# Kernel optimization log

Measured on AMD Instinct MI355X. Metric: run time of the kernel, lower is better.

Reference implementation:

```python
import jax, jax.numpy as jnp
import numpy as np

B, S, IN, OUT, P = 4, 1024, 128, 128, 16
CTX = min(IN, OUT)
MAX_SEQ = 4096


def setup_inputs() -> dict:
    key = jax.random.key(0)
    keys = iter(jax.random.split(key, 32))
    nk = lambda: next(keys)

    def linear(fi, fo):
        lim = 1.0 / np.sqrt(fi)
        W = jax.random.uniform(nk(), (fi, fo), jnp.float32, -lim, lim)
        b = jax.random.uniform(nk(), (fo,), jnp.float32, -lim, lim)
        return W, b

    x = jax.random.normal(nk(), (B, S, IN), jnp.float32)
    context_features = jax.random.normal(nk(), (B, S, CTX), jnp.float32)
    flow_patterns = jax.random.normal(nk(), (P, OUT, IN), jnp.float32) * 0.1
    w_sel1, b_sel1 = linear(IN + CTX, 2 * P)
    w_sel2, b_sel2 = linear(2 * P, P)
    w_int1, b_int1 = linear(IN + CTX, 64)
    w_int2, b_int2 = linear(64, 1)
    w_win1, b_win1 = linear(IN, 64)
    w_win2, b_win2 = linear(64, 1)
    return dict(x=x, context_features=context_features, flow_patterns=flow_patterns,
                w_sel1=w_sel1, b_sel1=b_sel1, w_sel2=w_sel2, b_sel2=b_sel2,
                w_int1=w_int1, b_int1=b_int1, w_int2=w_int2, b_int2=b_int2,
                w_win1=w_win1, b_win1=b_win1, w_win2=w_win2, b_win2=b_win2)


def _gelu(v):
    return jax.nn.gelu(v, approximate=False)  # torch nn.GELU default (erf)


def reference(x, context_features, flow_patterns,
              w_sel1, b_sel1, w_sel2, b_sel2,
              w_int1, b_int1, w_int2, b_int2,
              w_win1, b_win1, w_win2, b_win2):
    # combined input [B,S,IN+CTX]
    combined = jnp.concatenate([x, context_features], axis=-1)
    # pattern weights [B,S,P]
    pattern_weights = jax.nn.softmax(_gelu(combined @ w_sel1 + b_sel1) @ w_sel2 + b_sel2, axis=-1)
    # per-token flow matrix [B,S,OUT,IN]
    flow = jnp.einsum('bsp,poi->bsoi', pattern_weights, flow_patterns)
    # flow intensity [B,S,1] -> [B,S,1,1]
    intensity = jax.nn.sigmoid(_gelu(combined @ w_int1 + b_int1) @ w_int2 + b_int2)
    flow = flow * intensity[..., None]
    # adaptive window size [B,1]
    window_size = jax.nn.sigmoid(_gelu(x.mean(axis=1) @ w_win1 + b_win1) @ w_win2 + b_win2)
    window_size = window_size * (MAX_SEQ - 256) + 256
    # context-aware topk sparsity over flattened out*in dim
    adaptive_sparsity = 0.1 * jnp.mean(window_size / MAX_SEQ)  # scalar
    D = OUT * IN
    k = jnp.maximum(1, jnp.floor(D * adaptive_sparsity)).astype(jnp.int32)
    flat = flow.reshape(B, S, D)
    a = jnp.abs(flat)
    sorted_a = jnp.sort(a, axis=-1)  # ascending
    # k-th largest abs value per (b,s) row; k is a traced scalar -> dynamic_slice
    thr = jax.lax.dynamic_slice_in_dim(sorted_a, D - k, 1, axis=-1)  # [B,S,1]
    mask = jax.lax.stop_gradient((a >= thr).astype(flat.dtype))
    return (mask * flat).reshape(B, S, OUT, IN)
```

## Files before the change

kernel.cpp:

```cpp
#include <hip/hip_runtime.h>
#include <math.h>

#define S_   1024
#define D_   16384
#define CAPL 512
#define NB   512

typedef float v4f __attribute__((ext_vector_type(4)));

__device__ __forceinline__ double gelu64(double v) {
    return 0.5 * v * (1.0 + erf(v * 0.70710678118654752440));
}
__device__ __forceinline__ float gelu32(float v) {
    return 0.5f * v * (1.0f + erff(v * 0.70710678f));
}
__device__ __forceinline__ double sigmoid64(double z) {
    return 1.0 / (1.0 + exp(-z));
}
__device__ __forceinline__ float sigmoid32(float z) {
    return 1.0f / (1.0f + expf(-z));
}
__device__ __forceinline__ float rfl(float x) {
    return __uint_as_float(__builtin_amdgcn_readfirstlane(__float_as_uint(x)));
}

__global__ __launch_bounds__(256) void mlp_kernel(
    const float* __restrict__ x, const float* __restrict__ ctx,
    const float* __restrict__ w_sel1, const float* __restrict__ b_sel1,
    const float* __restrict__ w_sel2, const float* __restrict__ b_sel2,
    const float* __restrict__ w_int1, const float* __restrict__ b_int1,
    const float* __restrict__ w_int2, const float* __restrict__ b_int2,
    double* __restrict__ pw64, float* __restrict__ pw32,
    double* __restrict__ it64, float* __restrict__ it32)
{
    __shared__ double comb[2][256];
    __shared__ double h1[2][32];
    __shared__ float ipart[2][2];
    const int tid = threadIdx.x;
    const int tok0 = blockIdx.x * 2;
    const int t = tid >> 7, local = tid & 127;

    for (int r = 0; r < 2; ++r) {
        int idx = tid + r * 256;
        int tk = idx >> 8, i = idx & 255;
        comb[tk][i] = (double)((i < 128) ? x[(tok0 + tk) * 128 + i]
                                         : ctx[(tok0 + tk) * 128 + (i - 128)]);
    }
    __syncthreads();

    {
        int u = local >> 2, sl = local & 3;
        int i0 = sl * 64;
        double s0 = (sl == 0) ? (double)b_sel1[u] : 0.0, s1 = 0.0;
        for (int i = 0; i < 64; i += 2) {
            s0 = fma(comb[t][i0 + i],     (double)w_sel1[(i0 + i) * 32 + u],     s0);
            s1 = fma(comb[t][i0 + i + 1], (double)w_sel1[(i0 + i + 1) * 32 + u], s1);
        }
        double s = s0 + s1;
        s += __shfl_xor(s, 1);
        s += __shfl_xor(s, 2);
        if (sl == 0) h1[t][u] = gelu64(s);
    }
    {
        int u = local >> 1, sl = local & 1;
        int i0 = sl * 128;
        float a0 = (sl == 0) ? b_int1[u] : 0.0f, a1 = 0.0f, a2 = 0.0f, a3 = 0.0f;
        for (int i = 0; i < 128; i += 4) {
            a0 = fmaf((float)comb[t][i0 + i],     w_int1[(i0 + i) * 64 + u],     a0);
            a1 = fmaf((float)comb[t][i0 + i + 1], w_int1[(i0 + i + 1) * 64 + u], a1);
            a2 = fmaf((float)comb[t][i0 + i + 2], w_int1[(i0 + i + 2) * 64 + u], a2);
            a3 = fmaf((float)comb[t][i0 + i + 3], w_int1[(i0 + i + 3) * 64 + u], a3);
        }
        float s = (a0 + a1) + (a2 + a3);
        s += __shfl_xor(s, 1);
        float val = (sl == 0) ? gelu32(s) * w_int2[u] : 0.0f;
        for (int off = 2; off <= 32; off <<= 1)
            val += __shfl_xor(val, off);
        val += __shfl_xor(val, 1);
        if ((local & 63) == 0) ipart[t][local >> 6] = val;
    }
    __syncthreads();

    if (tid < 32) {
        int t2 = tid >> 4, u = tid & 15;
        double z = (double)b_sel2[u];
        for (int j = 0; j < 32; ++j)
            z = fma(h1[t2][j], (double)w_sel2[j * 16 + u], z);
        double m = z;
        for (int off = 8; off >= 1; off >>= 1) m = fmax(m, __shfl_xor(m, off));
        double e = exp(z - m);
        double ssum = e;
        for (int off = 8; off >= 1; off >>= 1) ssum += __shfl_xor(ssum, off);
        double pwv = e / ssum;
        pw64[(tok0 + t2) * 16 + u] = pwv;
        pw32[(tok0 + t2) * 16 + u] = (float)pwv;
    } else if (tid < 34) {
        int t3 = tid - 32;
        float iv = sigmoid32(ipart[t3][0] + ipart[t3][1] + b_int2[0]);
        it64[tok0 + t3] = (double)iv;
        it32[tok0 + t3] = iv;
    }
}

__global__ __launch_bounds__(256) void win_part_kernel(
    const float* __restrict__ x, double* __restrict__ wpart)
{
    __shared__ double red[2][128];
    const int tid = threadIdx.x;
    const int b = blockIdx.x >> 4, chunk = blockIdx.x & 15;
    int i = tid & 127, h = tid >> 7;
    double a0 = 0.0, a1 = 0.0;
    int s0 = b * S_ + chunk * 64 + h * 32;
    for (int j = 0; j < 32; j += 2) {
        a0 += (double)x[(s0 + j) * 128 + i];
        a1 += (double)x[(s0 + j + 1) * 128 + i];
    }
    red[h][i] = a0 + a1;
    __syncthreads();
    if (tid < 128)
        wpart[(b * 16 + chunk) * 128 + tid] = red[0][tid] + red[1][tid];
}

__global__ __launch_bounds__(256) void win_fin_kernel(
    const double* __restrict__ wpart,
    const float* __restrict__ w_win1, const float* __restrict__ b_win1,
    const float* __restrict__ w_win2, const float* __restrict__ b_win2,
    double* __restrict__ win_out)
{
    __shared__ double xm[4][128];
    const int tid = threadIdx.x;
    const int b = tid >> 6, lane = tid & 63;
    for (int r = 0; r < 2; ++r) {
        int i = lane + r * 64;
        double s = 0.0;
        for (int c = 0; c < 16; ++c)
            s += wpart[(b * 16 + c) * 128 + i];
        xm[b][i] = s * (1.0 / 1024.0);
    }
    __syncthreads();
    {
        int u = lane;
        double s0 = (double)b_win1[u], s1 = 0.0;
        for (int i = 0; i < 128; i += 2) {
            s0 = fma(xm[b][i],     (double)w_win1[i * 64 + u],       s0);
            s1 = fma(xm[b][i + 1], (double)w_win1[(i + 1) * 64 + u], s1);
        }
        double c = gelu64(s0 + s1) * (double)w_win2[u];
        for (int off = 32; off >= 1; off >>= 1) c += __shfl_xor(c, off);
        if (lane == 0)
            win_out[b] = sigmoid64(c + (double)b_win2[0]) * 3840.0 + 256.0;
    }
}

__global__ __launch_bounds__(512, 4) void flow_kernel(
    const float* __restrict__ patterns,
    const double* __restrict__ pw64, const float* __restrict__ pw32,
    const double* __restrict__ it64, const float* __restrict__ it32,
    const double* __restrict__ win,
    float* __restrict__ out)
{
    __shared__ unsigned hist[2][NB];
    __shared__ unsigned flagBits[2][512];
    __shared__ unsigned listIdx[2][CAPL];
    __shared__ double listVal[2][CAPL];
    __shared__ float smax[2][8];
    __shared__ int sred[8];
    __shared__ int bcastB[2];
    __shared__ unsigned listCnt[2];

    const int tid = threadIdx.x;
    const int lane = tid & 63, wv = tid >> 6;
    const int t0 = blockIdx.x * 2, t1 = t0 + 1;

    for (int r = tid; r < 2 * NB; r += 512) hist[r >> 9][r & (NB - 1)] = 0;
    for (int r = tid; r < 1024; r += 512) flagBits[r >> 9][r & 511] = 0;
    if (tid < 2) listCnt[tid] = 0;

    double w0 = win[0] * (1.0 / 4096.0), w1 = win[1] * (1.0 / 4096.0);
    double w2 = win[2] * (1.0 / 4096.0), w3 = win[3] * (1.0 / 4096.0);
    double mean = (((w0 + w1) + w2) + w3) * 0.25;
    double kd = floor(16384.0 * (0.1 * mean));
    int k = (kd < 1.0) ? 1 : (int)kd;

    float qw0[16], qw1[16];
#pragma unroll
    for (int p = 0; p < 16; ++p) {
        qw0[p] = rfl(pw32[t0 * 16 + p]);
        qw1[p] = rfl(pw32[t1 * 16 + p]);
    }
    float i0 = rfl(it32[t0]), i1 = rfl(it32[t1]);

    const v4f* pat4 = (const v4f*)patterns;
    v4f v0[8], v1[8];
#pragma unroll
    for (int c = 0; c < 8; ++c) {
        int grp = c * 512 + tid;
        v4f a0 = (v4f)(0.0f), a1 = (v4f)(0.0f);
        v4f pp[8];
#pragma unroll
        for (int p = 0; p < 8; ++p) pp[p] = pat4[p * 4096 + grp];
#pragma unroll
        for (int p = 0; p < 8; ++p) { a0 += qw0[p] * pp[p]; a1 += qw1[p] * pp[p]; }
#pragma unroll
        for (int p = 0; p < 8; ++p) pp[p] = pat4[(8 + p) * 4096 + grp];
#pragma unroll
        for (int p = 0; p < 8; ++p) { a0 += qw0[8 + p] * pp[p]; a1 += qw1[8 + p] * pp[p]; }
        v0[c] = a0 * i0;
        v1[c] = a1 * i1;
    }

    float mx0 = 0.0f, mx1 = 0.0f;
#pragma unroll
    for (int c = 0; c < 8; ++c) {
        mx0 = fmaxf(mx0, fmaxf(fmaxf(fabsf(v0[c].x), fabsf(v0[c].y)),
                               fmaxf(fabsf(v0[c].z), fabsf(v0[c].w))));
        mx1 = fmaxf(mx1, fmaxf(fmaxf(fabsf(v1[c].x), fabsf(v1[c].y)),
                               fmaxf(fabsf(v1[c].z), fabsf(v1[c].w))));
    }
    for (int off = 32; off >= 1; off >>= 1) {
        mx0 = fmaxf(mx0, __shfl_xor(mx0, off));
        mx1 = fmaxf(mx1, __shfl_xor(mx1, off));
    }
    if (lane == 0) { smax[0][wv] = mx0; smax[1][wv] = mx1; }
    __syncthreads();
    mx0 = smax[0][0]; mx1 = smax[1][0];
#pragma unroll
    for (int w = 1; w < 8; ++w) {
        mx0 = fmaxf(mx0, smax[0][w]);
        mx1 = fmaxf(mx1, smax[1][w]);
    }
    int base0 = (int)(__float_as_uint(mx0) >> 17) - (NB - 1);
    int base1 = (int)(__float_as_uint(mx1) >> 17) - (NB - 1);
    if (base0 < 0) base0 = 0;
    if (base1 < 0) base1 = 0;

#pragma unroll
    for (int c = 0; c < 8; ++c) {
#pragma unroll
        for (int q = 0; q < 4; ++q) {
            int b0 = (int)(__float_as_uint(fabsf(v0[c][q])) >> 17) - base0;
            if (b0 > 0) atomicAdd(&hist[0][b0 > NB - 1 ? NB - 1 : b0], 1u);
            int b1 = (int)(__float_as_uint(fabsf(v1[c][q])) >> 17) - base1;
            if (b1 > 0) atomicAdd(&hist[1][b1 > NB - 1 ? NB - 1 : b1], 1u);
        }
    }
    __syncthreads();

    if (wv < 2) {
        int t = wv;
        int sum8 = 0;
#pragma unroll
        for (int j = 0; j < 8; ++j) sum8 += (int)hist[t][lane * 8 + j];
        int suffix = sum8;
        for (int off = 1; off <= 32; off <<= 1) {
            int other = __shfl_down(suffix, off);
            if (lane + off < 64) suffix += other;
        }
        int sufNext = __shfl_down(suffix, 1);
        if (lane == 63) sufNext = 0;
        unsigned long long msk = __ballot(suffix >= k);
        int Lstar = (msk == 0) ? 0 : (63 - __clzll(msk));
        if (lane == Lstar) {
            int cnt = sufNext, B = Lstar * 8;
            for (int j = 7; j >= 0; --j) {
                cnt += (int)hist[t][Lstar * 8 + j];
                if (cnt >= k) { B = Lstar * 8 + j; break; }
            }
            bcastB[t] = B;
        }
    }
    __syncthreads();

    int B0 = bcastB[0], B1 = bcastB[1];
    float loF0 = (B0 + base0) ? __uint_as_float((unsigned)(B0 + base0) << 17) : 0.0f;
    float hiF0 = __uint_as_float((unsigned)(B0 + base0 + 1) << 17);
    float loF1 = (B1 + base1) ? __uint_as_float((unsigned)(B1 + base1) << 17) : 0.0f;
    float hiF1 = __uint_as_float((unsigned)(B1 + base1 + 1) << 17);

    float E0 = 3e-6f * i0, E1 = 3e-6f * i1;
    float loCut0 = loF0 - 2.0f * E0, hiCut0 = hiF0 + 2.0f * E0;
    float loCut1 = loF1 - 2.0f * E1, hiCut1 = hiF1 + 2.0f * E1;

    int ns0 = 0, ns1 = 0;
#pragma unroll
    for (int c = 0; c < 8; ++c) {
#pragma unroll
        for (int q = 0; q < 4; ++q) {
            unsigned e = (unsigned)(4 * (c * 512 + tid) + q);
            float a0 = fabsf(v0[c][q]);
            if (a0 >= hiCut0) ns0++;
            else if (a0 >= loCut0) {
                unsigned pos = atomicAdd(&listCnt[0], 1u);
                if (pos < CAPL) listIdx[0][pos] = e;
            }
            float a1 = fabsf(v1[c][q]);
            if (a1 >= hiCut1) ns1++;
            else if (a1 >= loCut1) {
                unsigned pos = atomicAdd(&listCnt[1], 1u);
                if (pos < CAPL) listIdx[1][pos] = e;
            }
        }
    }
    {
        int pk = ns0 | (ns1 << 16);
#pragma unroll
        for (int off = 32; off >= 1; off >>= 1) pk += __shfl_xor(pk, off);
        if (lane == 0) sred[wv] = pk;
    }
    __syncthreads();
    int tot = 0;
#pragma unroll
    for (int w = 0; w < 8; ++w) tot += sred[w];
    int m0 = k - (tot & 0xffff), m1 = k - (tot >> 16);
    int c0n = (int)(listCnt[0] < CAPL ? listCnt[0] : CAPL);
    int c1n = (int)(listCnt[1] < CAPL ? listCnt[1] : CAPL);

    double itt0 = it64[t0], itt1 = it64[t1];
    int totL = c0n + c1n;
    for (int g = tid; g < totL; g += 512) {
        int tk = (g >= c0n);
        int e = tk ? (g - c0n) : g;
        unsigned idx = listIdx[tk][e];
        const double* pwp = pw64 + (tk ? t1 : t0) * 16;
        double s = 0.0;
#pragma unroll
        for (int p = 0; p < 16; ++p)
            s = fma(pwp[p], (double)patterns[p * D_ + idx], s);
        listVal[tk][e] = fabs(s * (tk ? itt1 : itt0));
    }
    __syncthreads();
    for (int g = tid; g < totL; g += 512) {
        int tk = (g >= c0n);
        int e = tk ? (g - c0n) : g;
        double my = listVal[tk][e];
        int cnt = tk ? c1n : c0n, m = tk ? m1 : m0;
        int r = 0;
        for (int j = 0; j < cnt; ++j) r += (listVal[tk][j] > my);
        if (r < m) {
            unsigned idx = listIdx[tk][e];
            atomicOr(&flagBits[tk][idx >> 5], 1u << (idx & 31));
        }
    }
    __syncthreads();

    v4f* o0p = (v4f*)(out + (size_t)t0 * D_);
    v4f* o1p = (v4f*)(out + (size_t)t1 * D_);
#pragma unroll
    for (int c = 0; c < 8; ++c) {
        int grp = c * 512 + tid;
        v4f r0, r1;
#pragma unroll
        for (int q = 0; q < 4; ++q) {
            unsigned e = (unsigned)(4 * grp + q);
            float av = fabsf(v0[c][q]);
            bool keep = (av >= hiCut0);
            if (!keep && av >= loCut0) keep = (flagBits[0][e >> 5] >> (e & 31)) & 1u;
            r0[q] = keep ? v0[c][q] : 0.0f;
            av = fabsf(v1[c][q]);
            keep = (av >= hiCut1);
            if (!keep && av >= loCut1) keep = (flagBits[1][e >> 5] >> (e & 31)) & 1u;
            r1[q] = keep ? v1[c][q] : 0.0f;
        }
        __builtin_nontemporal_store(r0, &o0p[grp]);
        __builtin_nontemporal_store(r1, &o1p[grp]);
    }
}

extern "C" void kernel_launch(void* const* d_in, const int* in_sizes, int n_in,
                              void* d_out, int out_size, void* d_ws, size_t ws_size,
                              hipStream_t stream) {
    const float* x        = (const float*)d_in[0];
    const float* ctx      = (const float*)d_in[1];
    const float* patterns = (const float*)d_in[2];
    const float* w_sel1   = (const float*)d_in[3];
    const float* b_sel1   = (const float*)d_in[4];
    const float* w_sel2   = (const float*)d_in[5];
    const float* b_sel2   = (const float*)d_in[6];
    const float* w_int1   = (const float*)d_in[7];
    const float* b_int1   = (const float*)d_in[8];
    const float* w_int2   = (const float*)d_in[9];
    const float* b_int2   = (const float*)d_in[10];
    const float* w_win1   = (const float*)d_in[11];
    const float* b_win1   = (const float*)d_in[12];
    const float* w_win2   = (const float*)d_in[13];
    const float* b_win2   = (const float*)d_in[14];

    double* ws    = (double*)d_ws;
    double* win   = ws;
    double* pw64  = ws + 8;
    double* it64  = pw64 + 65536;
    double* wpart = it64 + 4096;
    float*  pw32  = (float*)(wpart + 8192);
    float*  it32  = pw32 + 65536;
    float*  out   = (float*)d_out;

    hipLaunchKernelGGL(mlp_kernel, dim3(2048), dim3(256), 0, stream,
                       x, ctx, w_sel1, b_sel1, w_sel2, b_sel2,
                       w_int1, b_int1, w_int2, b_int2, pw64, pw32, it64, it32);
    hipLaunchKernelGGL(win_part_kernel, dim3(64), dim3(256), 0, stream, x, wpart);
    hipLaunchKernelGGL(win_fin_kernel, dim3(1), dim3(256), 0, stream,
                       wpart, w_win1, b_win1, w_win2, b_win2, win);
    hipLaunchKernelGGL(flow_kernel, dim3(2048), dim3(512), 0, stream,
                       patterns, pw64, pw32, it64, it32, win, out);
}
```

Measured before the change: 441.3 us.

## Process four tokens per block in flow kernel to reuse pattern loads

The flow kernel now handles four tokens per block instead of two, so each pattern load is shared across four accumulations. This halves the grid and the total pattern-read traffic through cache. Register pressure doubles (four 32-element vectors per thread), so launch bounds drop to 2 blocks per CU. The refine stage now assumes each list fits in one pass of 512 threads, and the shared-memory footprint grows.

```diff
diff --git a/kernel.cpp b/kernel.cpp
--- a/kernel.cpp
+++ b/kernel.cpp
@@ -152,29 +152,29 @@
     }
 }
 
-__global__ __launch_bounds__(512, 4) void flow_kernel(
+__global__ __launch_bounds__(512, 2) void flow_kernel(
     const float* __restrict__ patterns,
     const double* __restrict__ pw64, const float* __restrict__ pw32,
     const double* __restrict__ it64, const float* __restrict__ it32,
     const double* __restrict__ win,
     float* __restrict__ out)
 {
-    __shared__ unsigned hist[2][NB];
-    __shared__ unsigned flagBits[2][512];
-    __shared__ unsigned listIdx[2][CAPL];
-    __shared__ double listVal[2][CAPL];
-    __shared__ float smax[2][8];
+    __shared__ unsigned hist[4][NB];
+    __shared__ unsigned flagBits[4][512];
+    __shared__ unsigned listIdx[4][CAPL];
+    __shared__ double listVal[4][CAPL];
+    __shared__ float smax[4][8];
     __shared__ int sred[8];
-    __shared__ int bcastB[2];
-    __shared__ unsigned listCnt[2];
+    __shared__ int bcastB[4];
+    __shared__ unsigned listCnt[4];
 
     const int tid = threadIdx.x;
     const int lane = tid & 63, wv = tid >> 6;
-    const int t0 = blockIdx.x * 2, t1 = t0 + 1;
-
-    for (int r = tid; r < 2 * NB; r += 512) hist[r >> 9][r & (NB - 1)] = 0;
-    for (int r = tid; r < 1024; r += 512) flagBits[r >> 9][r & 511] = 0;
-    if (tid < 2) listCnt[tid] = 0;
+    const int t0 = blockIdx.x * 4;
+
+    for (int r = tid; r < 4 * NB; r += 512) hist[r >> 9][r & (NB - 1)] = 0;
+    for (int r = tid; r < 2048; r += 512) flagBits[r >> 9][r & 511] = 0;
+    if (tid < 4) listCnt[tid] = 0;
 
     double w0 = win[0] * (1.0 / 4096.0), w1 = win[1] * (1.0 / 4096.0);
     double w2 = win[2] * (1.0 / 4096.0), w3 = win[3] * (1.0 / 4096.0);
@@ -182,71 +182,98 @@
     double kd = floor(16384.0 * (0.1 * mean));
     int k = (kd < 1.0) ? 1 : (int)kd;
 
-    float qw0[16], qw1[16];
+    float qw0[16], qw1[16], qw2[16], qw3[16];
 #pragma unroll
     for (int p = 0; p < 16; ++p) {
-        qw0[p] = rfl(pw32[t0 * 16 + p]);
-        qw1[p] = rfl(pw32[t1 * 16 + p]);
-    }
-    float i0 = rfl(it32[t0]), i1 = rfl(it32[t1]);
+        qw0[p] = rfl(pw32[(t0 + 0) * 16 + p]);
+        qw1[p] = rfl(pw32[(t0 + 1) * 16 + p]);
+        qw2[p] = pw32[(t0 + 2) * 16 + p];
+        qw3[p] = pw32[(t0 + 3) * 16 + p];
+    }
+    float it0 = rfl(it32[t0 + 0]), it1 = rfl(it32[t0 + 1]);
+    float it2 = it32[t0 + 2],      it3 = it32[t0 + 3];
 
     const v4f* pat4 = (const v4f*)patterns;
-    v4f v0[8], v1[8];
+    v4f v0[8], v1[8], v2[8], v3[8];
 #pragma unroll
     for (int c = 0; c < 8; ++c) {
         int grp = c * 512 + tid;
-        v4f a0 = (v4f)(0.0f), a1 = (v4f)(0.0f);
+        v4f a0 = (v4f)(0.0f), a1 = (v4f)(0.0f), a2 = (v4f)(0.0f), a3 = (v4f)(0.0f);
         v4f pp[8];
 #pragma unroll
         for (int p = 0; p < 8; ++p) pp[p] = pat4[p * 4096 + grp];
 #pragma unroll
-        for (int p = 0; p < 8; ++p) { a0 += qw0[p] * pp[p]; a1 += qw1[p] * pp[p]; }
+        for (int p = 0; p < 8; ++p) {
+            a0 += qw0[p] * pp[p]; a1 += qw1[p] * pp[p];
+            a2 += qw2[p] * pp[p]; a3 += qw3[p] * pp[p];
+        }
 #pragma unroll
         for (int p = 0; p < 8; ++p) pp[p] = pat4[(8 + p) * 4096 + grp];
 #pragma unroll
-        for (int p = 0; p < 8; ++p) { a0 += qw0[8 + p] * pp[p]; a1 += qw1[8 + p] * pp[p]; }
-        v0[c] = a0 * i0;
-        v1[c] = a1 * i1;
-    }
-
-    float mx0 = 0.0f, mx1 = 0.0f;
+        for (int p = 0; p < 8; ++p) {
+            a0 += qw0[8 + p] * pp[p]; a1 += qw1[8 + p] * pp[p];
+            a2 += qw2[8 + p] * pp[p]; a3 += qw3[8 + p] * pp[p];
+        }
+        v0[c] = a0 * it0; v1[c] = a1 * it1;
+        v2[c] = a2 * it2; v3[c] = a3 * it3;
+    }
+
+    float mx0 = 0.0f, mx1 = 0.0f, mx2 = 0.0f, mx3 = 0.0f;
 #pragma unroll
     for (int c = 0; c < 8; ++c) {
         mx0 = fmaxf(mx0, fmaxf(fmaxf(fabsf(v0[c].x), fabsf(v0[c].y)),
                                fmaxf(fabsf(v0[c].z), fabsf(v0[c].w))));
         mx1 = fmaxf(mx1, fmaxf(fmaxf(fabsf(v1[c].x), fabsf(v1[c].y)),
                                fmaxf(fabsf(v1[c].z), fabsf(v1[c].w))));
+        mx2 = fmaxf(mx2, fmaxf(fmaxf(fabsf(v2[c].x), fabsf(v2[c].y)),
+                               fmaxf(fabsf(v2[c].z), fabsf(v2[c].w))));
+        mx3 = fmaxf(mx3, fmaxf(fmaxf(fabsf(v3[c].x), fabsf(v3[c].y)),
+                               fmaxf(fabsf(v3[c].z), fabsf(v3[c].w))));
     }
     for (int off = 32; off >= 1; off >>= 1) {
         mx0 = fmaxf(mx0, __shfl_xor(mx0, off));
         mx1 = fmaxf(mx1, __shfl_xor(mx1, off));
-    }
-    if (lane == 0) { smax[0][wv] = mx0; smax[1][wv] = mx1; }
-    __syncthreads();
-    mx0 = smax[0][0]; mx1 = smax[1][0];
-#pragma unroll
-    for (int w = 1; w < 8; ++w) {
-        mx0 = fmaxf(mx0, smax[0][w]);
-        mx1 = fmaxf(mx1, smax[1][w]);
-    }
-    int base0 = (int)(__float_as_uint(mx0) >> 17) - (NB - 1);
-    int base1 = (int)(__float_as_uint(mx1) >> 17) - (NB - 1);
-    if (base0 < 0) base0 = 0;
-    if (base1 < 0) base1 = 0;
+        mx2 = fmaxf(mx2, __shfl_xor(mx2, off));
+        mx3 = fmaxf(mx3, __shfl_xor(mx3, off));
+    }
+    if (lane == 0) {
+        smax[0][wv] = mx0; smax[1][wv] = mx1;
+        smax[2][wv] = mx2; smax[3][wv] = mx3;
+    }
+    __syncthreads();
+    int base[4];
+    {
+        float m0 = smax[0][0], m1 = smax[1][0], m2 = smax[2][0], m3 = smax[3][0];
+#pragma unroll
+        for (int w = 1; w < 8; ++w) {
+            m0 = fmaxf(m0, smax[0][w]); m1 = fmaxf(m1, smax[1][w]);
+            m2 = fmaxf(m2, smax[2][w]); m3 = fmaxf(m3, smax[3][w]);
+        }
+        int b0 = (int)(__float_as_uint(m0) >> 17) - (NB - 1);
+        int b1 = (int)(__float_as_uint(m1) >> 17) - (NB - 1);
+        int b2 = (int)(__float_as_uint(m2) >> 17) - (NB - 1);
+        int b3 = (int)(__float_as_uint(m3) >> 17) - (NB - 1);
+        base[0] = (b0 < 0) ? 0 : b0; base[1] = (b1 < 0) ? 0 : b1;
+        base[2] = (b2 < 0) ? 0 : b2; base[3] = (b3 < 0) ? 0 : b3;
+    }
 
 #pragma unroll
     for (int c = 0; c < 8; ++c) {
 #pragma unroll
         for (int q = 0; q < 4; ++q) {
-            int b0 = (int)(__float_as_uint(fabsf(v0[c][q])) >> 17) - base0;
+            int b0 = (int)(__float_as_uint(fabsf(v0[c][q])) >> 17) - base[0];
             if (b0 > 0) atomicAdd(&hist[0][b0 > NB - 1 ? NB - 1 : b0], 1u);
-            int b1 = (int)(__float_as_uint(fabsf(v1[c][q])) >> 17) - base1;
+            int b1 = (int)(__float_as_uint(fabsf(v1[c][q])) >> 17) - base[1];
             if (b1 > 0) atomicAdd(&hist[1][b1 > NB - 1 ? NB - 1 : b1], 1u);
-        }
-    }
-    __syncthreads();
-
-    if (wv < 2) {
+            int b2 = (int)(__float_as_uint(fabsf(v2[c][q])) >> 17) - base[2];
+            if (b2 > 0) atomicAdd(&hist[2][b2 > NB - 1 ? NB - 1 : b2], 1u);
+            int b3 = (int)(__float_as_uint(fabsf(v3[c][q])) >> 17) - base[3];
+            if (b3 > 0) atomicAdd(&hist[3][b3 > NB - 1 ? NB - 1 : b3], 1u);
+        }
+    }
+    __syncthreads();
+
+    if (wv < 4) {
         int t = wv;
         int sum8 = 0;
 #pragma unroll
@@ -271,98 +298,138 @@
     }
     __syncthreads();
 
-    int B0 = bcastB[0], B1 = bcastB[1];
-    float loF0 = (B0 + base0) ? __uint_as_float((unsigned)(B0 + base0) << 17) : 0.0f;
-    float hiF0 = __uint_as_float((unsigned)(B0 + base0 + 1) << 17);
-    float loF1 = (B1 + base1) ? __uint_as_float((unsigned)(B1 + base1) << 17) : 0.0f;
-    float hiF1 = __uint_as_float((unsigned)(B1 + base1 + 1) << 17);
-
-    float E0 = 3e-6f * i0, E1 = 3e-6f * i1;
-    float loCut0 = loF0 - 2.0f * E0, hiCut0 = hiF0 + 2.0f * E0;
-    float loCut1 = loF1 - 2.0f * E1, hiCut1 = hiF1 + 2.0f * E1;
-
-    int ns0 = 0, ns1 = 0;
+    float loCut[4], hiCut[4];
+    float itArr[4] = {it0, it1, it2, it3};
+#pragma unroll
+    for (int t = 0; t < 4; ++t) {
+        int B = bcastB[t];
+        float loF = (B + base[t]) ? __uint_as_float((unsigned)(B + base[t]) << 17) : 0.0f;
+        float hiF = __uint_as_float((unsigned)(B + base[t] + 1) << 17);
+        float E = 3e-6f * itArr[t];
+        loCut[t] = loF - 2.0f * E;
+        hiCut[t] = hiF + 2.0f * E;
+    }
+
+    int ns0 = 0, ns1 = 0, ns2 = 0, ns3 = 0;
 #pragma unroll
     for (int c = 0; c < 8; ++c) {
 #pragma unroll
         for (int q = 0; q < 4; ++q) {
             unsigned e = (unsigned)(4 * (c * 512 + tid) + q);
-            float a0 = fabsf(v0[c][q]);
-            if (a0 >= hiCut0) ns0++;
-            else if (a0 >= loCut0) {
+            float a;
+            a = fabsf(v0[c][q]);
+            if (a >= hiCut[0]) ns0++;
+            else if (a >= loCut[0]) {
                 unsigned pos = atomicAdd(&listCnt[0], 1u);
                 if (pos < CAPL) listIdx[0][pos] = e;
             }
-            float a1 = fabsf(v1[c][q]);
-            if (a1 >= hiCut1) ns1++;
-            else if (a1 >= loCut1) {
+            a = fabsf(v1[c][q]);
+            if (a >= hiCut[1]) ns1++;
+            else if (a >= loCut[1]) {
                 unsigned pos = atomicAdd(&listCnt[1], 1u);
                 if (pos < CAPL) listIdx[1][pos] = e;
             }
-        }
-    }
+            a = fabsf(v2[c][q]);
+            if (a >= hiCut[2]) ns2++;
+            else if (a >= loCut[2]) {
+                unsigned pos = atomicAdd(&listCnt[2], 1u);
+                if (pos < CAPL) listIdx[2][pos] = e;
+            }
+            a = fabsf(v3[c][q]);
+            if (a >= hiCut[3]) ns3++;
+            else if (a >= loCut[3]) {
+                unsigned pos = atomicAdd(&listCnt[3], 1u);
+                if (pos < CAPL) listIdx[3][pos] = e;
+            }
+        }
+    }
+    int m[4];
     {
-        int pk = ns0 | (ns1 << 16);
-#pragma unroll
-        for (int off = 32; off >= 1; off >>= 1) pk += __shfl_xor(pk, off);
-        if (lane == 0) sred[wv] = pk;
-    }
-    __syncthreads();
-    int tot = 0;
-#pragma unroll
-    for (int w = 0; w < 8; ++w) tot += sred[w];
-    int m0 = k - (tot & 0xffff), m1 = k - (tot >> 16);
-    int c0n = (int)(listCnt[0] < CAPL ? listCnt[0] : CAPL);
-    int c1n = (int)(listCnt[1] < CAPL ? listCnt[1] : CAPL);
-
-    double itt0 = it64[t0], itt1 = it64[t1];
-    int totL = c0n + c1n;
-    for (int g = tid; g < totL; g += 512) {
-        int tk = (g >= c0n);
-        int e = tk ? (g - c0n) : g;
-        unsigned idx = listIdx[tk][e];
-        const double* pwp = pw64 + (tk ? t1 : t0) * 16;
-        double s = 0.0;
-#pragma unroll
-        for (int p = 0; p < 16; ++p)
-            s = fma(pwp[p], (double)patterns[p * D_ + idx], s);
-        listVal[tk][e] = fabs(s * (tk ? itt1 : itt0));
-    }
-    __syncthreads();
-    for (int g = tid; g < totL; g += 512) {
-        int tk = (g >= c0n);
-        int e = tk ? (g - c0n) : g;
-        double my = listVal[tk][e];
-        int cnt = tk ? c1n : c0n, m = tk ? m1 : m0;
-        int r = 0;
-        for (int j = 0; j < cnt; ++j) r += (listVal[tk][j] > my);
-        if (r < m) {
-            unsigned idx = listIdx[tk][e];
-            atomicOr(&flagBits[tk][idx >> 5], 1u << (idx & 31));
-        }
-    }
-    __syncthreads();
-
-    v4f* o0p = (v4f*)(out + (size_t)t0 * D_);
-    v4f* o1p = (v4f*)(out + (size_t)t1 * D_);
+        int pk01 = ns0 | (ns1 << 16);
+        int pk23 = ns2 | (ns3 << 16);
+#pragma unroll
+        for (int off = 32; off >= 1; off >>= 1) {
+            pk01 += __shfl_xor(pk01, off);
+            pk23 += __shfl_xor(pk23, off);
+        }
+        if (lane == 0) { sred[wv] = pk01; }
+        __syncthreads();
+        int tot01 = 0;
+#pragma unroll
+        for (int w = 0; w < 8; ++w) tot01 += sred[w];
+        __syncthreads();
+        if (lane == 0) { sred[wv] = pk23; }
+        __syncthreads();
+        int tot23 = 0;
+#pragma unroll
+        for (int w = 0; w < 8; ++w) tot23 += sred[w];
+        m[0] = k - (tot01 & 0xffff); m[1] = k - (tot01 >> 16);
+        m[2] = k - (tot23 & 0xffff); m[3] = k - (tot23 >> 16);
+    }
+    int cn[4];
+#pragma unroll
+    for (int t = 0; t < 4; ++t)
+        cn[t] = (int)(listCnt[t] < CAPL ? listCnt[t] : CAPL);
+
+#pragma unroll
+    for (int t = 0; t < 4; ++t) {
+        if (tid < cn[t]) {
+            unsigned idx = listIdx[t][tid];
+            const double* pwp = pw64 + (size_t)(t0 + t) * 16;
+            double itt = it64[t0 + t];
+            double s = 0.0;
+#pragma unroll
+            for (int p = 0; p < 16; ++p)
+                s = fma(pwp[p], (double)patterns[p * D_ + idx], s);
+            listVal[t][tid] = fabs(s * itt);
+        }
+    }
+    __syncthreads();
+#pragma unroll
+    for (int t = 0; t < 4; ++t) {
+        if (tid < cn[t]) {
+            double my = listVal[t][tid];
+            int r = 0;
+            for (int j = 0; j < cn[t]; ++j) r += (listVal[t][j] > my);
+            if (r < m[t]) {
+                unsigned idx = listIdx[t][tid];
+                atomicOr(&flagBits[t][idx >> 5], 1u << (idx & 31));
+            }
+        }
+    }
+    __syncthreads();
+
 #pragma unroll
     for (int c = 0; c < 8; ++c) {
         int grp = c * 512 + tid;
-        v4f r0, r1;
+        v4f r0, r1, r2, r3;
 #pragma unroll
         for (int q = 0; q < 4; ++q) {
             unsigned e = (unsigned)(4 * grp + q);
-            float av = fabsf(v0[c][q]);
-            bool keep = (av >= hiCut0);
-            if (!keep && av >= loCut0) keep = (flagBits[0][e >> 5] >> (e & 31)) & 1u;
+            unsigned w = e >> 5, bm = 1u << (e & 31);
+            float av;
+            bool keep;
+            av = fabsf(v0[c][q]);
+            keep = (av >= hiCut[0]);
+            if (!keep && av >= loCut[0]) keep = (flagBits[0][w] & bm) != 0;
             r0[q] = keep ? v0[c][q] : 0.0f;
             av = fabsf(v1[c][q]);
-            keep = (av >= hiCut1);
-            if (!keep && av >= loCut1) keep = (flagBits[1][e >> 5] >> (e & 31)) & 1u;
+            keep = (av >= hiCut[1]);
+            if (!keep && av >= loCut[1]) keep = (flagBits[1][w] & bm) != 0;
             r1[q] = keep ? v1[c][q] : 0.0f;
-        }
-        __builtin_nontemporal_store(r0, &o0p[grp]);
-        __builtin_nontemporal_store(r1, &o1p[grp]);
+            av = fabsf(v2[c][q]);
+            keep = (av >= hiCut[2]);
+            if (!keep && av >= loCut[2]) keep = (flagBits[2][w] & bm) != 0;
+            r2[q] = keep ? v2[c][q] : 0.0f;
+            av = fabsf(v3[c][q]);
+            keep = (av >= hiCut[3]);
+            if (!keep && av >= loCut[3]) keep = (flagBits[3][w] & bm) != 0;
+            r3[q] = keep ? v3[c][q] : 0.0f;
+        }
+        __builtin_nontemporal_store(r0, (v4f*)(out + (size_t)(t0 + 0) * D_) + grp);
+        __builtin_nontemporal_store(r1, (v4f*)(out + (size_t)(t0 + 1) * D_) + grp);
+        __builtin_nontemporal_store(r2, (v4f*)(out + (size_t)(t0 + 2) * D_) + grp);
+        __builtin_nontemporal_store(r3, (v4f*)(out + (size_t)(t0 + 3) * D_) + grp);
     }
 }
 
@@ -400,6 +467,6 @@
     hipLaunchKernelGGL(win_part_kernel, dim3(64), dim3(256), 0, stream, x, wpart);
     hipLaunchKernelGGL(win_fin_kernel, dim3(1), dim3(256), 0, stream,
                        wpart, w_win1, b_win1, w_win2, b_win2, win);
-    hipLaunchKernelGGL(flow_kernel, dim3(2048), dim3(512), 0, stream,
+    hipLaunchKernelGGL(flow_kernel, dim3(1024), dim3(512), 0, stream,
                        patterns, pw64, pw32, it64, it32, win, out);
 }
```

Result: slower. 536.9 us (+21.7%).
